# Kernel tuning notes

Measured on AMD Instinct MI355X. Metric: run time of the kernel, lower is better.

The kernel has to match this reference:

```python
import jax, jax.numpy as jnp
import numpy as np

N = 8192
IN_F = 512
OUT_F = 512
ALPHA = 0.2  # leaky relu slope


def setup_inputs() -> dict:
    key = jax.random.key(0)
    k1, k2, k3, k4, k5 = jax.random.split(key, 5)
    inp = jax.random.normal(k1, (N, IN_F), dtype=jnp.float32)
    adj = jax.random.randint(k2, (N, N), 0, 2, dtype=jnp.int32)
    # linear1: [in, out] + bias
    W1 = jax.random.normal(k3, (IN_F, OUT_F), dtype=jnp.float32) * (1.0 / np.sqrt(IN_F))
    b1 = jnp.zeros((OUT_F,), dtype=jnp.float32)
    # linear2: maps 2*out -> 1; split into the two halves acting on h_i and h_j
    a = jax.random.normal(k4, (2 * OUT_F,), dtype=jnp.float32) * (1.0 / np.sqrt(2 * OUT_F))
    a1 = a[:OUT_F]
    a2 = a[OUT_F:]
    b2 = jnp.zeros((), dtype=jnp.float32)
    return {"inp": inp, "adj": adj, "W1": W1, "b1": b1, "a1": a1, "a2": a2, "b2": b2}


def reference(inp, adj, W1, b1, a1, a2, b2):
    h = inp @ W1 + b1  # [N, out]
    # linear2(cat(h_i, h_j)) == h_i@a1 + h_j@a2 + b2 -> avoids the N*N*2F tensor
    e = jax.nn.leaky_relu((h @ a1)[:, None] + (h @ a2)[None, :] + b2, ALPHA)  # [N, N]
    attention = jnp.where(adj > 0, e, jnp.float32(-1e12))
    attention = jax.nn.softmax(attention, axis=1)
    h_prime = attention @ h  # [N, out]
    return jax.nn.elu(h_prime)  # concat=True
```

## Files before the change

kernel.cpp:

```cpp
#include <hip/hip_runtime.h>
#include <hip/hip_bf16.h>
#include <stdint.h>

#define NR 8192
#define FD 512
#define BM 64

typedef __attribute__((ext_vector_type(8))) short s8v;
typedef __attribute__((ext_vector_type(4))) float f32x4;

static __device__ __forceinline__ short bf16_rtne(float x) {
    union { float f; uint32_t u; } v; v.f = x;
    uint32_t r = (v.u + 0x7FFFu + ((v.u >> 16) & 1u)) >> 16;
    return (short)r;
}
static __device__ __forceinline__ float bf16_to_f32(short s) {
    union { uint32_t u; float f; } v; v.u = ((uint32_t)(uint16_t)s) << 16;
    return v.f;
}

__global__ void k_prep(const float* __restrict__ in, short* __restrict__ out,
                       const float* __restrict__ W1, short* __restrict__ W1T) {
    int b = blockIdx.x;
    if (b < 4096) {
        int i = b * 256 + threadIdx.x;
        float4 v = ((const float4*)in)[i];
        short4 s;
        s.x = bf16_rtne(v.x); s.y = bf16_rtne(v.y);
        s.z = bf16_rtne(v.z); s.w = bf16_rtne(v.w);
        ((short4*)out)[i] = s;
    } else {
        int i = (b - 4096) * 256 + threadIdx.x;
        int k = i & 511, n = i >> 9;
        W1T[(size_t)n * 512 + k] = bf16_rtne(W1[(size_t)k * 512 + n]);
    }
}

__launch_bounds__(256)
__global__ void k_gemm_h(const short* __restrict__ A,
                         const short* __restrict__ BT,
                         const float* __restrict__ b1,
                         short* __restrict__ H,
                         short* __restrict__ HT3)
{
    const int lane = threadIdx.x & 63;
    const int wn   = threadIdx.x >> 6;
    const int m    = lane & 15;
    const int q    = lane >> 4;
    const int r0   = blockIdx.x * 32;
    const int c0   = blockIdx.y * 128 + wn * 32;

    f32x4 acc[2][2] = {};
#pragma unroll 1
    for (int k0 = 0; k0 < 512; k0 += 32) {
        s8v a[2], b[2];
#pragma unroll
        for (int rt = 0; rt < 2; ++rt)
            a[rt] = *(const s8v*)(A + (size_t)(r0 + rt * 16 + m) * 512 + k0 + q * 8);
#pragma unroll
        for (int nt = 0; nt < 2; ++nt)
            b[nt] = *(const s8v*)(BT + (size_t)(c0 + nt * 16 + m) * 512 + k0 + q * 8);
#pragma unroll
        for (int rt = 0; rt < 2; ++rt)
#pragma unroll
            for (int nt = 0; nt < 2; ++nt)
                acc[rt][nt] = __builtin_amdgcn_mfma_f32_16x16x32_bf16(a[rt], b[nt], acc[rt][nt], 0, 0, 0);
    }
    float b1v[2];
#pragma unroll
    for (int nt = 0; nt < 2; ++nt) b1v[nt] = b1[c0 + nt * 16 + m];

#pragma unroll
    for (int rt = 0; rt < 2; ++rt)
#pragma unroll
        for (int nt = 0; nt < 2; ++nt) {
            int col = c0 + nt * 16 + m;
            short4 hp;
#pragma unroll
            for (int r = 0; r < 4; ++r) {
                int row = r0 + rt * 16 + q * 4 + r;
                short hv = bf16_rtne(acc[rt][nt][r] + b1v[nt]);
                H[(size_t)row * 512 + col] = hv;
                ((short*)&hp)[r] = hv;
            }
            size_t off = (size_t)blockIdx.x * 16384
                       + (size_t)(blockIdx.y * 2 + (wn >> 1)) * 2048
                       + (size_t)((wn * 2 + nt) & 3) * 512
                       + (rt * 2 + (q >> 1)) * 128
                       + m * 8 + (q & 1) * 4;
            *(short4*)(HT3 + off) = hp;
        }
}

__global__ void k_f1f2(const short* __restrict__ H, const float* __restrict__ a1,
                       const float* __restrict__ a2, const float* __restrict__ b2,
                       float* __restrict__ f1, float* __restrict__ f2s)
{
    const int lane = threadIdx.x & 63;
    const int row  = blockIdx.x * 4 + (threadIdx.x >> 6);
    s8v hv = *(const s8v*)(H + (size_t)row * 512 + lane * 8);
    float4 a1l = ((const float4*)(a1 + lane * 8))[0];
    float4 a1h = ((const float4*)(a1 + lane * 8))[1];
    float4 a2l = ((const float4*)(a2 + lane * 8))[0];
    float4 a2h = ((const float4*)(a2 + lane * 8))[1];
    float hf[8];
#pragma unroll
    for (int i = 0; i < 8; ++i) hf[i] = bf16_to_f32(hv[i]);
    float s1 = hf[0] * a1l.x + hf[1] * a1l.y + hf[2] * a1l.z + hf[3] * a1l.w
             + hf[4] * a1h.x + hf[5] * a1h.y + hf[6] * a1h.z + hf[7] * a1h.w;
    float s2 = hf[0] * a2l.x + hf[1] * a2l.y + hf[2] * a2l.z + hf[3] * a2l.w
             + hf[4] * a2h.x + hf[5] * a2h.y + hf[6] * a2h.z + hf[7] * a2h.w;
#pragma unroll
    for (int o = 32; o > 0; o >>= 1) {
        s1 += __shfl_xor(s1, o);
        s2 += __shfl_xor(s2, o);
    }
    if (lane == 0) {
        f1[row]  = s1;
        f2s[row] = s2 + b2[0];
    }
}

__launch_bounds__(1024, 4)
__global__ void k_attn(const int* __restrict__ adj,
                       const short* __restrict__ HT3,
                       const float* __restrict__ f1,
                       const float* __restrict__ f2s,
                       float* __restrict__ nump,
                       float* __restrict__ denomp)
{
    __shared__ __align__(16) short wt[2][BM * 256];

    const int t    = threadIdx.x;
    const int lane = t & 63;
    const int w    = t >> 6;
    const int m    = lane & 15;
    const int q    = lane >> 4;

    const int js   = blockIdx.x & 1;
    const int band = blockIdx.x >> 1;
    const int r0   = band * BM;
    const int jb0  = js * 4096;
    const int jt0  = js * 128;

    const int prow = t >> 4;
    const int jg   = t & 15;

    const float f1v = f1[r0 + prow];
    const int* adjrow = adj + (size_t)(r0 + prow) * NR + jb0;
    const float* f2base = f2s + jb0;

    f32x4 acc[4][2] = {};
    float dsum = 0.f;

#define GAT_BLOAD(DST, KT)                                                     \
    {                                                                          \
        const short* s_ = HT3 + (size_t)(jt0 + (KT)) * 16384 + (w >> 1) * 2048 \
                        + (w & 1) * 1024 + q * 128 + m * 8;                    \
        DST[0] = *(const s8v*)(s_);                                            \
        DST[1] = *(const s8v*)(s_ + 512);                                      \
    }

#define GAT_MRAW(DA, DB, AP, U)                                                \
    {                                                                          \
        DA = *(const uint4*)((AP) + (U) * 8);                                  \
        DB = *(const uint4*)((AP) + (U) * 8 + 4);                              \
    }

#define GAT_MPACK(DST, MA, MB)                                                 \
    {                                                                          \
        DST = ((int)(MA).x > 0 ? 1u : 0u)  | ((int)(MA).y > 0 ? 2u : 0u)       \
            | ((int)(MA).z > 0 ? 4u : 0u)  | ((int)(MA).w > 0 ? 8u : 0u)       \
            | ((int)(MB).x > 0 ? 16u : 0u) | ((int)(MB).y > 0 ? 32u : 0u)      \
            | ((int)(MB).z > 0 ? 64u : 0u) | ((int)(MB).w > 0 ? 128u : 0u);    \
    }

#define GAT_WUNIT(U, BYTE, FA, FB, P)                                          \
    {                                                                          \
        s8v wv_;                                                               \
        const float* ff_ = (const float*)&(FA);                                \
        _Pragma("unroll")                                                      \
        for (int jj = 0; jj < 4; ++jj) {                                       \
            float s_ = f1v + ff_[jj];                                          \
            float e_ = __expf(fmaxf(s_, 0.2f * s_));                           \
            float x_ = (((BYTE) >> jj) & 1u) ? e_ : 0.f;                       \
            dsum += x_; wv_[jj] = bf16_rtne(x_);                               \
        }                                                                      \
        const float* fg_ = (const float*)&(FB);                               \
        _Pragma("unroll")                                                      \
        for (int jj = 0; jj < 4; ++jj) {                                       \
            float s_ = f1v + fg_[jj];                                          \
            float e_ = __expf(fmaxf(s_, 0.2f * s_));                           \
            float x_ = (((BYTE) >> (4 + jj)) & 1u) ? e_ : 0.f;                 \
            dsum += x_; wv_[4 + jj] = bf16_rtne(x_);                           \
        }                                                                      \
        *(s8v*)&wt[P][prow * 256 + (((U) ^ (prow & 7)) << 3)] = wv_;           \
    }

    {
#pragma unroll
        for (int k_ = 0; k_ < 2; ++k_) {
            const int u_ = jg + 16 * k_;
            uint4 pa_, pb_;
            GAT_MRAW(pa_, pb_, adjrow, u_)
            uint32_t mk_;
            GAT_MPACK(mk_, pa_, pb_)
            float4 fa_ = *(const float4*)(f2base + u_ * 8);
            float4 fb_ = *(const float4*)(f2base + u_ * 8 + 4);
            GAT_WUNIT(u_, mk_, fa_, fb_, 0)
        }
    }
    s8v breg[4][2];
    GAT_BLOAD(breg[0], 0)
    GAT_BLOAD(breg[1], 1)
    __syncthreads();

    int kt = 0;
#pragma unroll 1
    for (int ch = 0; ch < 16; ++ch) {
        const int p = ch & 1;
        const int chn = (ch + 1) & 15;
        const int* adjn = adjrow + chn * 256;
        const float* f2n = f2base + chn * 256;
        uint4 m0a, m0b, m1a, m1b;
        uint32_t mk0, mk1;
        float4 fa0, fb0, fa1, fb1;
        const int u0 = jg;
        const int u1 = jg + 16;

#pragma unroll
        for (int kk = 0; kk < 8; ++kk, ++kt) {
            GAT_BLOAD(breg[(kk + 2) & 3], (kt + 2) & 127)
            if (ch < 15) {
                if (kk == 0) {
                    GAT_MRAW(m0a, m0b, adjn, u0)
                    fa0 = *(const float4*)(f2n + u0 * 8);
                    fb0 = *(const float4*)(f2n + u0 * 8 + 4);
                } else if (kk == 1) {
                    GAT_MRAW(m1a, m1b, adjn, u1)
                    fa1 = *(const float4*)(f2n + u1 * 8);
                    fb1 = *(const float4*)(f2n + u1 * 8 + 4);
                }
            }
            s8v af[4];
#pragma unroll
            for (int i = 0; i < 4; ++i)
                af[i] = *(const s8v*)&wt[p][(i * 16 + m) * 256
                                            + (((kk * 4 + q) ^ (m & 7)) << 3)];
            __builtin_amdgcn_s_setprio(1);
#pragma unroll
            for (int nt = 0; nt < 2; ++nt)
#pragma unroll
                for (int i = 0; i < 4; ++i)
                    acc[i][nt] = __builtin_amdgcn_mfma_f32_16x16x32_bf16(af[i], breg[kk & 3][nt], acc[i][nt], 0, 0, 0);
            __builtin_amdgcn_s_setprio(0);
            if (ch < 15) {
                if (kk == 2)      { GAT_MPACK(mk0, m0a, m0b) }
                else if (kk == 3) { GAT_MPACK(mk1, m1a, m1b) }
                else if (kk == 4) { GAT_WUNIT(u0, mk0, fa0, fb0, p ^ 1) }
                else if (kk == 5) { GAT_WUNIT(u1, mk1, fa1, fb1, p ^ 1) }
            }
        }
        __syncthreads();
    }
#undef GAT_BLOAD
#undef GAT_MRAW
#undef GAT_MPACK
#undef GAT_WUNIT

    dsum += __shfl_xor(dsum, 1);
    dsum += __shfl_xor(dsum, 2);
    dsum += __shfl_xor(dsum, 4);
    dsum += __shfl_xor(dsum, 8);
    if (jg == 0) denomp[(size_t)js * NR + r0 + prow] = dsum;

    float* np = nump + (size_t)js * NR * FD;
#pragma unroll
    for (int i = 0; i < 4; ++i)
#pragma unroll
        for (int nt = 0; nt < 2; ++nt)
#pragma unroll
            for (int r = 0; r < 4; ++r) {
                int row = r0 + i * 16 + q * 4 + r;
                int col = w * 32 + nt * 16 + m;
                np[(size_t)row * FD + col] = acc[i][nt][r];
            }
}

__global__ void k_combine(const float* __restrict__ nump,
                          const float* __restrict__ denomp,
                          float* __restrict__ out)
{
    size_t e = ((size_t)blockIdx.x * 256 + threadIdx.x) * 4;
    int row = (int)(e >> 9);
    float4 n0 = *(const float4*)(nump + e);
    float4 n1 = *(const float4*)(nump + (size_t)NR * FD + e);
    float d = denomp[row] + denomp[NR + row];
    float inv = 1.0f / d;
    float4 o;
    o.x = (n0.x + n1.x) * inv;
    o.y = (n0.y + n1.y) * inv;
    o.z = (n0.z + n1.z) * inv;
    o.w = (n0.w + n1.w) * inv;
    o.x = (o.x > 0.f) ? o.x : (__expf(o.x) - 1.f);
    o.y = (o.y > 0.f) ? o.y : (__expf(o.y) - 1.f);
    o.z = (o.z > 0.f) ? o.z : (__expf(o.z) - 1.f);
    o.w = (o.w > 0.f) ? o.w : (__expf(o.w) - 1.f);
    *(float4*)(out + e) = o;
}

extern "C" void kernel_launch(void* const* d_in, const int* in_sizes, int n_in,
                              void* d_out, int out_size, void* d_ws, size_t ws_size,
                              hipStream_t stream) {
    const float* inp = (const float*)d_in[0];
    const int*   adj = (const int*)d_in[1];
    const float* W1  = (const float*)d_in[2];
    const float* b1  = (const float*)d_in[3];
    const float* a1  = (const float*)d_in[4];
    const float* a2  = (const float*)d_in[5];
    const float* b2  = (const float*)d_in[6];
    float* out = (float*)d_out;

    short*    inp_bf = (short*)d_ws;
    short*    w1t    = inp_bf + (size_t)NR * FD;
    short*    h      = w1t + (size_t)FD * FD;
    short*    ht3    = h + (size_t)NR * FD;
    float*    f1     = (float*)(ht3 + (size_t)FD * NR);
    float*    f2s    = f1 + NR;
    float*    nump   = f2s + NR;
    float*    denomp = nump + (size_t)2 * NR * FD;

    k_prep<<<4096 + 1024, 256, 0, stream>>>(inp, inp_bf, W1, w1t);
    dim3 g1(NR / 32, FD / 128);
    k_gemm_h<<<g1, 256, 0, stream>>>(inp_bf, w1t, b1, h, ht3);
    k_f1f2<<<NR / 4, 256, 0, stream>>>(h, a1, a2, b2, f1, f2s);
    k_attn<<<128 * 2, 1024, 0, stream>>>(adj, ht3, f1, f2s, nump, denomp);
    k_combine<<<(NR * FD / 4) / 256, 256, 0, stream>>>(nump, denomp, out);
}
```

Measured before the change: 500.5 us.

## Halve attention row band to 32 with 512-thread blocks and deeper adjacency prefetch

```diff
diff --git a/kernel.cpp b/kernel.cpp
--- a/kernel.cpp
+++ b/kernel.cpp
@@ -4,7 +4,7 @@
 
 #define NR 8192
 #define FD 512
-#define BM 64
+#define BM 32
 
 typedef __attribute__((ext_vector_type(8))) short s8v;
 typedef __attribute__((ext_vector_type(4))) float f32x4;
@@ -121,13 +121,14 @@
     }
 }
 
-__launch_bounds__(1024, 4)
-__global__ void k_attn(const int* __restrict__ adj,
-                       const short* __restrict__ HT3,
-                       const float* __restrict__ f1,
-                       const float* __restrict__ f2s,
-                       float* __restrict__ nump,
-                       float* __restrict__ denomp)
+__global__ __attribute__((amdgpu_flat_work_group_size(512, 512)))
+           __attribute__((amdgpu_waves_per_eu(4, 4)))
+void k_attn(const int* __restrict__ adj,
+            const short* __restrict__ HT3,
+            const float* __restrict__ f1,
+            const float* __restrict__ f2s,
+            float* __restrict__ nump,
+            float* __restrict__ denomp)
 {
     __shared__ __align__(16) short wt[2][BM * 256];
 
@@ -150,15 +151,17 @@
     const int* adjrow = adj + (size_t)(r0 + prow) * NR + jb0;
     const float* f2base = f2s + jb0;
 
-    f32x4 acc[4][2] = {};
+    f32x4 acc[2][4] = {};
     float dsum = 0.f;
 
 #define GAT_BLOAD(DST, KT)                                                     \
     {                                                                          \
-        const short* s_ = HT3 + (size_t)(jt0 + (KT)) * 16384 + (w >> 1) * 2048 \
-                        + (w & 1) * 1024 + q * 128 + m * 8;                    \
+        const short* s_ = HT3 + (size_t)(jt0 + (KT)) * 16384 + w * 2048        \
+                        + q * 128 + m * 8;                                     \
         DST[0] = *(const s8v*)(s_);                                            \
         DST[1] = *(const s8v*)(s_ + 512);                                      \
+        DST[2] = *(const s8v*)(s_ + 1024);                                     \
+        DST[3] = *(const s8v*)(s_ + 1536);                                     \
     }
 
 #define GAT_MRAW(DA, DB, AP, U)                                                \
@@ -197,6 +200,7 @@
         *(s8v*)&wt[P][prow * 256 + (((U) ^ (prow & 7)) << 3)] = wv_;           \
     }
 
+    uint32_t mkB0 = 0, mkB1 = 0;
     {
 #pragma unroll
         for (int k_ = 0; k_ < 2; ++k_) {
@@ -209,8 +213,13 @@
             float4 fb_ = *(const float4*)(f2base + u_ * 8 + 4);
             GAT_WUNIT(u_, mk_, fa_, fb_, 0)
         }
-    }
-    s8v breg[4][2];
+        uint4 pa_, pb_;
+        GAT_MRAW(pa_, pb_, adjrow + 256, jg)
+        GAT_MPACK(mkB0, pa_, pb_)
+        GAT_MRAW(pa_, pb_, adjrow + 256, jg + 16)
+        GAT_MPACK(mkB1, pa_, pb_)
+    }
+    s8v breg[2][4];
     GAT_BLOAD(breg[0], 0)
     GAT_BLOAD(breg[1], 1)
     __syncthreads();
@@ -219,48 +228,56 @@
 #pragma unroll 1
     for (int ch = 0; ch < 16; ++ch) {
         const int p = ch & 1;
-        const int chn = (ch + 1) & 15;
-        const int* adjn = adjrow + chn * 256;
-        const float* f2n = f2base + chn * 256;
-        uint4 m0a, m0b, m1a, m1b;
-        uint32_t mk0, mk1;
+        const int ch1 = (ch + 1) & 15;
+        const int ch2 = (ch + 2) & 15;
+        const int* adj2 = adjrow + ch2 * 256;
+        const float* f2n = f2base + ch1 * 256;
+        uint4 r0a, r0b, r1a, r1b;
+        uint32_t mkA0 = 0, mkA1 = 0;
         float4 fa0, fb0, fa1, fb1;
-        const int u0 = jg;
-        const int u1 = jg + 16;
 
 #pragma unroll
         for (int kk = 0; kk < 8; ++kk, ++kt) {
-            GAT_BLOAD(breg[(kk + 2) & 3], (kt + 2) & 127)
+            const int e = kk & 1;
+            s8v bn[4];
+            GAT_BLOAD(bn, (kt + 2) & 127)
+            if (ch < 14) {
+                if (kk == 0)      { GAT_MRAW(r0a, r0b, adj2, jg) }
+                else if (kk == 1) { GAT_MRAW(r1a, r1b, adj2, jg + 16) }
+            }
             if (ch < 15) {
-                if (kk == 0) {
-                    GAT_MRAW(m0a, m0b, adjn, u0)
-                    fa0 = *(const float4*)(f2n + u0 * 8);
-                    fb0 = *(const float4*)(f2n + u0 * 8 + 4);
-                } else if (kk == 1) {
-                    GAT_MRAW(m1a, m1b, adjn, u1)
-                    fa1 = *(const float4*)(f2n + u1 * 8);
-                    fb1 = *(const float4*)(f2n + u1 * 8 + 4);
+                if (kk == 2) {
+                    fa0 = *(const float4*)(f2n + jg * 8);
+                    fb0 = *(const float4*)(f2n + jg * 8 + 4);
+                } else if (kk == 3) {
+                    fa1 = *(const float4*)(f2n + (jg + 16) * 8);
+                    fb1 = *(const float4*)(f2n + (jg + 16) * 8 + 4);
                 }
             }
-            s8v af[4];
-#pragma unroll
-            for (int i = 0; i < 4; ++i)
+            s8v af[2];
+#pragma unroll
+            for (int i = 0; i < 2; ++i)
                 af[i] = *(const s8v*)&wt[p][(i * 16 + m) * 256
                                             + (((kk * 4 + q) ^ (m & 7)) << 3)];
             __builtin_amdgcn_s_setprio(1);
 #pragma unroll
-            for (int nt = 0; nt < 2; ++nt)
-#pragma unroll
-                for (int i = 0; i < 4; ++i)
-                    acc[i][nt] = __builtin_amdgcn_mfma_f32_16x16x32_bf16(af[i], breg[kk & 3][nt], acc[i][nt], 0, 0, 0);
+            for (int nt = 0; nt < 4; ++nt)
+#pragma unroll
+                for (int i = 0; i < 2; ++i)
+                    acc[i][nt] = __builtin_amdgcn_mfma_f32_16x16x32_bf16(af[i], breg[e][nt], acc[i][nt], 0, 0, 0);
             __builtin_amdgcn_s_setprio(0);
+            if (ch < 14) {
+                if (kk == 3)      { GAT_MPACK(mkA0, r0a, r0b) }
+                else if (kk == 4) { GAT_MPACK(mkA1, r1a, r1b) }
+            }
             if (ch < 15) {
-                if (kk == 2)      { GAT_MPACK(mk0, m0a, m0b) }
-                else if (kk == 3) { GAT_MPACK(mk1, m1a, m1b) }
-                else if (kk == 4) { GAT_WUNIT(u0, mk0, fa0, fb0, p ^ 1) }
-                else if (kk == 5) { GAT_WUNIT(u1, mk1, fa1, fb1, p ^ 1) }
-            }
+                if (kk == 4)      { GAT_WUNIT(jg,      mkB0, fa0, fb0, p ^ 1) }
+                else if (kk == 5) { GAT_WUNIT(jg + 16, mkB1, fa1, fb1, p ^ 1) }
+            }
+#pragma unroll
+            for (int nt = 0; nt < 4; ++nt) breg[e][nt] = bn[nt];
         }
+        mkB0 = mkA0; mkB1 = mkA1;
         __syncthreads();
     }
 #undef GAT_BLOAD
@@ -276,13 +293,13 @@
 
     float* np = nump + (size_t)js * NR * FD;
 #pragma unroll
-    for (int i = 0; i < 4; ++i)
-#pragma unroll
-        for (int nt = 0; nt < 2; ++nt)
+    for (int i = 0; i < 2; ++i)
+#pragma unroll
+        for (int nt = 0; nt < 4; ++nt)
 #pragma unroll
             for (int r = 0; r < 4; ++r) {
                 int row = r0 + i * 16 + q * 4 + r;
-                int col = w * 32 + nt * 16 + m;
+                int col = w * 64 + nt * 16 + m;
                 np[(size_t)row * FD + col] = acc[i][nt][r];
             }
 }
@@ -334,6 +351,6 @@
     dim3 g1(NR / 32, FD / 128);
     k_gemm_h<<<g1, 256, 0, stream>>>(inp_bf, w1t, b1, h, ht3);
     k_f1f2<<<NR / 4, 256, 0, stream>>>(h, a1, a2, b2, f1, f2s);
-    k_attn<<<128 * 2, 1024, 0, stream>>>(adj, ht3, f1, f2s, nump, denomp);
+    k_attn<<<256 * 2, 512, 0, stream>>>(adj, ht3, f1, f2s, nump, denomp);
     k_combine<<<(NR * FD / 4) / 256, 256, 0, stream>>>(nump, denomp, out);
 }
```

Result: slower. 603.3 us (+20.5%).
